# Kernel tuning notes

Measured on AMD Instinct MI355X. Metric: run time of the kernel, lower is better.

## Reference

```python
import jax, jax.numpy as jnp
import numpy as np

T = 2048          # tokens (flattened prefill)
H = 3584          # hidden_size
NH = 16           # num query heads
NKV = 8           # num kv heads
G = NH // NKV     # GQA group size
D = 256           # head_dim
SCALE = 256.0 ** -0.5   # query_pre_attn_scalar ** -0.5
WINDOW = 1024     # sliding_window_size
CAP = 50.0        # logit softcap
BASE = 10000.0    # rope theta
NEG = -1e30


def _rope(x, positions):
    # x: [T, n, D], neox-style rotary over full head_dim
    half = D // 2
    inv_freq = 1.0 / (BASE ** (jnp.arange(0, D, 2, dtype=jnp.float32) / D))  # [half]
    ang = positions.astype(jnp.float32)[:, None] * inv_freq  # [T, half]
    cos = jnp.cos(ang)[:, None, :]  # [T,1,half]
    sin = jnp.sin(ang)[:, None, :]
    x1, x2 = x[..., :half], x[..., half:]
    return jnp.concatenate([x1 * cos - x2 * sin, x2 * cos + x1 * sin], axis=-1)


def setup_inputs() -> dict:
    key = jax.random.key(0)
    ks = jax.random.split(key, 5)
    s = 0.02
    return {
        "hidden_states": jax.random.normal(ks[0], (T, H), dtype=jnp.float32),
        "Wq": jax.random.normal(ks[1], (H, NH * D), dtype=jnp.float32) * s,
        "Wk": jax.random.normal(ks[2], (H, NKV * D), dtype=jnp.float32) * s,
        "Wv": jax.random.normal(ks[3], (H, NKV * D), dtype=jnp.float32) * s,
        "Wo": jax.random.normal(ks[4], (NH * D, H), dtype=jnp.float32) * s,
        "positions": jnp.arange(T, dtype=jnp.int32),
    }


def reference(hidden_states, Wq, Wk, Wv, Wo, positions):
    q = (hidden_states @ Wq).reshape(T, NH, D)
    k = (hidden_states @ Wk).reshape(T, NKV, D)
    v = (hidden_states @ Wv).reshape(T, NKV, D)
    q = _rope(q, positions)
    k = _rope(k, positions)

    # GQA attention: group query heads over kv heads
    qg = (q * SCALE).reshape(T, NKV, G, D)
    scores = jnp.einsum('qhgd,khd->hgqk', qg, k)  # [NKV,G,T,T]
    scores = CAP * jnp.tanh(scores / CAP)         # logit softcap

    i = jnp.arange(T)[:, None]
    j = jnp.arange(T)[None, :]
    mask = (j <= i) & (i - j < WINDOW)            # causal + sliding window
    scores = jnp.where(mask, scores, NEG)

    p = jax.nn.softmax(scores, axis=-1)
    o = jnp.einsum('hgqk,khd->qhgd', p, v).reshape(T, NH * D)
    return o @ Wo
```

## Files before the change

kernel.cpp:

```cpp
#include <hip/hip_runtime.h>
#include <math.h>

typedef __attribute__((ext_vector_type(8))) __bf16 bf16x8;
typedef __attribute__((ext_vector_type(4))) __bf16 bf16x4;
typedef __attribute__((ext_vector_type(4))) float f32x4;

#define TSEQ 2048
#define HDIM 3584
#define NQH  16
#define NKVH 8
#define DH   256
#define WIN  1024
#define QKD  (NQH * DH)
#define KVD  (NKVH * DH)
#define QKVN 8192

#define MFMA __builtin_amdgcn_mfma_f32_16x16x32_bf16

__device__ __forceinline__ void gload_lds16(const void* g, void* l) {
  __builtin_amdgcn_global_load_lds(
      (const __attribute__((address_space(1))) void*)g,
      (__attribute__((address_space(3))) void*)l, 16, 0, 0);
}


__global__ void cvt_bf16_kernel(const float* __restrict__ in,
                                __bf16* __restrict__ out, long n) {
  long i = ((long)blockIdx.x * blockDim.x + threadIdx.x) * 4;
  if (i >= n) return;
  float4 v = *reinterpret_cast<const float4*>(in + i);
  bf16x4 o4;
  o4.x = (__bf16)v.x; o4.y = (__bf16)v.y; o4.z = (__bf16)v.z; o4.w = (__bf16)v.w;
  *reinterpret_cast<bf16x4*>(out + i) = o4;
}

__global__ void transpose_cvt_kernel(const float* __restrict__ in,
                                     __bf16* __restrict__ out, int R, int C) {
  __shared__ float tile[32][33];
  const int tx = threadIdx.x, ty = threadIdx.y;
  const int c0 = blockIdx.x * 32, r0 = blockIdx.y * 32;
#pragma unroll
  for (int i = 0; i < 4; ++i)
    tile[ty + i * 8][tx] = in[(size_t)(r0 + ty + i * 8) * C + (c0 + tx)];
  __syncthreads();
#pragma unroll
  for (int i = 0; i < 4; ++i)
    out[(size_t)(c0 + ty + i * 8) * R + (r0 + tx)] = (__bf16)tile[tx][ty + i * 8];
}

__global__ void transpose_bf16_kernel(const __bf16* __restrict__ in,
                                      __bf16* __restrict__ out, int ldin, int ldout) {
  __shared__ __bf16 tile[32][33];
  const int tx = threadIdx.x, ty = threadIdx.y;
  const int c0 = blockIdx.x * 32, r0 = blockIdx.y * 32;
#pragma unroll
  for (int i = 0; i < 4; ++i)
    tile[ty + i * 8][tx] = in[(size_t)(r0 + ty + i * 8) * ldin + (c0 + tx)];
  __syncthreads();
#pragma unroll
  for (int i = 0; i < 4; ++i)
    out[(size_t)(c0 + ty + i * 8) * ldout + (r0 + tx)] = tile[tx][ty + i * 8];
}

__global__ void rope_table_kernel(const int* __restrict__ positions,
                                  float* __restrict__ ct,
                                  float* __restrict__ st) {
  int i = blockIdx.x * blockDim.x + threadIdx.x;
  if (i >= TSEQ * 128) return;
  int t = i >> 7, j = i & 127;
  float invf = (float)exp((double)(-2 * j) * (9.210340371976184 / 256.0));
  float ang = (float)positions[t] * invf;
  ct[i] = cosf(ang);
  st[i] = sinf(ang);
}

__global__ void rope_apply_kernel(__bf16* __restrict__ x,
                                  const float* __restrict__ ct,
                                  const float* __restrict__ st,
                                  int heads, int ld, float scale, int total) {
  int i = blockIdx.x * blockDim.x + threadIdx.x;
  if (i >= total) return;
  int j = i & 127;
  int th = i >> 7;
  int t = th / heads;
  int head = th - t * heads;
  size_t base = (size_t)t * ld + head * DH + j;
  float x1 = (float)x[base], x2 = (float)x[base + 128];
  float c = ct[(t << 7) + j], s = st[(t << 7) + j];
  x[base]       = (__bf16)((x1 * c - x2 * s) * scale);
  x[base + 128] = (__bf16)((x2 * c + x1 * s) * scale);
}

__global__ void reduce2_kernel(const float* __restrict__ p0,
                               const float* __restrict__ p1,
                               float* __restrict__ out, int n4) {
  int stride = gridDim.x * blockDim.x;
  for (int i = blockIdx.x * blockDim.x + threadIdx.x; i < n4; i += stride) {
    float4 a = reinterpret_cast<const float4*>(p0)[i];
    float4 b = reinterpret_cast<const float4*>(p1)[i];
    a.x += b.x; a.y += b.y; a.z += b.z; a.w += b.w;
    reinterpret_cast<float4*>(out)[i] = a;
  }
}


__device__ __forceinline__ void stage_half(const __bf16* __restrict__ gbase,
                                           int row0, int ldg, int k0,
                                           __bf16* lds_half, int tid) {
  const int lane = tid & 63;
  const int w = tid >> 6;
  const int lr = lane >> 3;
  const int swzcol = ((lane & 7) ^ lr) << 3;
  const __bf16* g = gbase + (size_t)(row0 + w * 8 + lr) * ldg + k0 + swzcol;
  __bf16* l = lds_half + w * 512;
  gload_lds16(g, l);
  gload_lds16(g + (size_t)64 * ldg, l + 4096);
}

#define BAR __builtin_amdgcn_s_barrier()

#define RD_A(DST, BASE, MO)                                         \
  _Pragma("unroll")                                                 \
  for (int m_ = 0; m_ < 4; ++m_) {                                  \
    const __bf16* p_ = (BASE) + (((MO) + m_) * 16 + l15) * 64;      \
    DST[m_][0] = *(const bf16x8*)(p_ + kxa);                        \
    DST[m_][1] = *(const bf16x8*)(p_ + kxb);                        \
  }

#define RD_B(DST, BASE, NO)                                         \
  _Pragma("unroll")                                                 \
  for (int n_ = 0; n_ < 2; ++n_) {                                  \
    const __bf16* p_ = (BASE) + (bro + ((NO) + n_) * 16 + l15) * 64;\
    DST[n_][0] = *(const bf16x8*)(p_ + kxa);                        \
    DST[n_][1] = *(const bf16x8*)(p_ + kxb);                        \
  }

#define MQUAD(AF, BF, MO, NO)                                          \
  __builtin_amdgcn_s_setprio(1);                                       \
  _Pragma("unroll")                                                    \
  for (int m_ = 0; m_ < 4; ++m_)                                       \
    _Pragma("unroll")                                                  \
    for (int n_ = 0; n_ < 2; ++n_) {                                   \
      acc[(MO) + m_][(NO) + n_] =                                      \
          MFMA(AF[m_][0], BF[n_][0], acc[(MO) + m_][(NO) + n_], 0, 0, 0); \
      acc[(MO) + m_][(NO) + n_] =                                      \
          MFMA(AF[m_][1], BF[n_][1], acc[(MO) + m_][(NO) + n_], 0, 0, 0); \
    }                                                                  \
  __builtin_amdgcn_s_setprio(0);

template <typename CT>
__global__ __launch_bounds__(512, 2) void gemm256_kernel(
    const __bf16* __restrict__ A, const __bf16* __restrict__ B,
    CT* __restrict__ C, int lda, int Klen, int ldc, int nrc, size_t cstride) {
  __shared__ __bf16 lds[2][2][2][8192];

  const int nwg = gridDim.x;
  const int per = nwg >> 3;
  const int wg = (blockIdx.x & 7) * per + (blockIdx.x >> 3);
  const int kslice = wg / nrc;
  const int rem = wg - kslice * nrc;
  const int row0 = (rem & 7) * 256;
  const int col0 = (rem >> 3) * 256;
  const int k0 = kslice * Klen;
  CT* Cs = C + (size_t)kslice * cstride;

  const int tid = threadIdx.x;
  const int lane = tid & 63, w = tid >> 6;
  const int wr = w >> 2, wc = w & 3;
  const int l15 = lane & 15, lg = lane >> 4;
  const int swz = (lane & 7) << 3;
  const int kxa = (lg * 8) ^ swz;
  const int kxb = (32 + lg * 8) ^ swz;
  const int bro = (wc & 1) * 64;

  const __bf16* Ablk = A + (size_t)row0 * lda + k0;
  const __bf16* Bblk = B + (size_t)col0 * lda + k0;

  const __bf16* Ae = &lds[0][0][wr][0];
  const __bf16* Be = &lds[0][1][wc >> 1][0];
  const __bf16* Ao = &lds[1][0][wr][0];
  const __bf16* Bo = &lds[1][1][wc >> 1][0];

  f32x4 acc[8][4] = {};
  const int NT = Klen >> 6;
  const int NI = NT >> 1;

  stage_half(Ablk, 0,   lda, 0,  &lds[0][0][0][0], tid);
  stage_half(Ablk, 128, lda, 0,  &lds[0][0][1][0], tid);
  stage_half(Bblk, 0,   lda, 0,  &lds[0][1][0][0], tid);
  stage_half(Bblk, 128, lda, 0,  &lds[0][1][1][0], tid);
  stage_half(Ablk, 0,   lda, 64, &lds[1][0][0][0], tid);
  stage_half(Ablk, 128, lda, 64, &lds[1][0][1][0], tid);
  asm volatile("s_waitcnt vmcnt(4)" ::: "memory");
  BAR;

  bf16x8 a03[4][2], a47[4][2], b01[2][2], b23[2][2];

  for (int j = 0; j < NI; ++j) {
    const int e = 2 * j, o = 2 * j + 1;
    const bool last = (j == NI - 1);

    RD_A(a03, Ae, 0);
    RD_B(b01, Be, 0);
    stage_half(Bblk, 0, lda, o * 64, &lds[1][1][0][0], tid);
    asm volatile("s_waitcnt lgkmcnt(8)" ::: "memory");
    BAR; MQUAD(a03, b01, 0, 0); BAR;

    RD_A(a47, Ae, 4);
    stage_half(Bblk, 128, lda, o * 64, &lds[1][1][1][0], tid);
    BAR; MQUAD(a47, b01, 4, 0); BAR;

    RD_B(b23, Be, 2);
    if (!last) stage_half(Ablk, 0, lda, (e + 2) * 64, &lds[0][0][0][0], tid);
    BAR; MQUAD(a47, b23, 4, 2); BAR;

    if (!last) {
      stage_half(Ablk, 128, lda, (e + 2) * 64, &lds[0][0][1][0], tid);
      asm volatile("s_waitcnt vmcnt(4)" ::: "memory");
    } else {
      asm volatile("s_waitcnt vmcnt(0)" ::: "memory");
    }
    BAR; MQUAD(a03, b23, 0, 2); BAR;

    RD_A(a03, Ao, 0);
    RD_B(b01, Bo, 0);
    if (!last) stage_half(Bblk, 0, lda, (e + 2) * 64, &lds[0][1][0][0], tid);
    asm volatile("s_waitcnt lgkmcnt(8)" ::: "memory");
    BAR; MQUAD(a03, b01, 0, 0); BAR;

    RD_A(a47, Ao, 4);
    if (!last) stage_half(Bblk, 128, lda, (e + 2) * 64, &lds[0][1][1][0], tid);
    BAR; MQUAD(a47, b01, 4, 0); BAR;

    RD_B(b23, Bo, 2);
    if (!last) stage_half(Ablk, 0, lda, (o + 2) * 64, &lds[1][0][0][0], tid);
    BAR; MQUAD(a47, b23, 4, 2); BAR;

    if (!last) {
      stage_half(Ablk, 128, lda, (o + 2) * 64, &lds[1][0][1][0], tid);
      asm volatile("s_waitcnt vmcnt(4)" ::: "memory");
    }
    BAR; MQUAD(a03, b23, 0, 2); BAR;
  }

#pragma unroll
  for (int m = 0; m < 8; ++m)
#pragma unroll
    for (int n = 0; n < 4; ++n)
#pragma unroll
      for (int r = 0; r < 4; ++r) {
        int row = row0 + wr * 128 + m * 16 + lg * 4 + r;
        int col = col0 + wc * 64 + n * 16 + l15;
        Cs[(size_t)row * ldc + col] = (CT)acc[m][n][r];
      }
}

__global__ __launch_bounds__(256, 2) void attn_kernel(
    const __bf16* __restrict__ q, const __bf16* __restrict__ k,
    const __bf16* __restrict__ vt, __bf16* __restrict__ o) {
  __shared__ __bf16 Klds[64][264];
  __shared__ __bf16 Vlds[256][72];
  __shared__ __bf16 Plds[4][16][72];

  const int tid = threadIdx.x;
  const int wave = tid >> 6;
  const int lane = tid & 63;
  const int l16 = lane & 15;
  const int lg = lane >> 4;
  const int qh = blockIdx.y;
  const int h = qh >> 1;
  const int q0 = blockIdx.x << 6;
  const int qr = q0 + wave * 16;

  bf16x8 qf[8];
  {
    const __bf16* qp = q + (size_t)(qr + l16) * QKVN + qh * DH + lg * 8;
#pragma unroll
    for (int ds = 0; ds < 8; ++ds)
      qf[ds] = *reinterpret_cast<const bf16x8*>(qp + ds * 32);
  }

  f32x4 accO[16] = {};
  float l_run[4] = {0.f, 0.f, 0.f, 0.f};

  int t_lo = q0 - (WIN - 1);
  if (t_lo < 0) t_lo = 0;
  t_lo &= ~63;

  for (int t0 = t_lo; t0 <= q0; t0 += 64) {
    __syncthreads();
    {
      const __bf16* kg = k + (size_t)t0 * QKVN + h * DH;
#pragma unroll
      for (int it = 0; it < 8; ++it) {
        int c = tid + it * 256;
        int row = c >> 5, col = (c & 31) * 8;
        *reinterpret_cast<bf16x8*>(&Klds[row][col]) =
            *reinterpret_cast<const bf16x8*>(kg + (size_t)row * QKVN + col);
      }
      const __bf16* vg = vt + (size_t)(h * DH) * TSEQ + t0;
#pragma unroll
      for (int it = 0; it < 8; ++it) {
        int c = tid + it * 256;
        int row = c >> 3, col = (c & 7) * 8;
        *reinterpret_cast<bf16x8*>(&Vlds[row][col]) =
            *reinterpret_cast<const bf16x8*>(vg + (size_t)row * TSEQ + col);
      }
    }
    __syncthreads();

    f32x4 accS[4] = {};
    __builtin_amdgcn_s_setprio(1);
#pragma unroll
    for (int nt = 0; nt < 4; ++nt)
#pragma unroll
      for (int ds = 0; ds < 8; ++ds) {
        bf16x8 kf = *reinterpret_cast<const bf16x8*>(&Klds[nt * 16 + l16][ds * 32 + lg * 8]);
        accS[nt] = MFMA(qf[ds], kf, accS[nt], 0, 0, 0);
      }
    __builtin_amdgcn_s_setprio(0);

    float rs[4] = {0.f, 0.f, 0.f, 0.f};
#pragma unroll
    for (int nt = 0; nt < 4; ++nt) {
      int key = t0 + nt * 16 + l16;
#pragma unroll
      for (int r = 0; r < 4; ++r) {
        int row = qr + lg * 4 + r;
        float t = __expf(accS[nt][r] * 0.04f);
        float p = __expf(-100.0f / (t + 1.0f));
        bool valid = (key <= row) && (row - key < WIN);
        p = valid ? p : 0.f;
        rs[r] += p;
        Plds[wave][lg * 4 + r][nt * 16 + l16] = (__bf16)p;
      }
    }
#pragma unroll
    for (int off = 1; off < 16; off <<= 1)
#pragma unroll
      for (int r = 0; r < 4; ++r)
        rs[r] += __shfl_xor(rs[r], off);
#pragma unroll
    for (int r = 0; r < 4; ++r)
      l_run[r] += rs[r];

    __builtin_amdgcn_s_setprio(1);
#pragma unroll
    for (int ks = 0; ks < 2; ++ks) {
      bf16x8 pa = *reinterpret_cast<const bf16x8*>(&Plds[wave][l16][ks * 32 + lg * 8]);
#pragma unroll
      for (int nt2 = 0; nt2 < 16; ++nt2) {
        bf16x8 vb = *reinterpret_cast<const bf16x8*>(&Vlds[nt2 * 16 + l16][ks * 32 + lg * 8]);
        accO[nt2] = MFMA(pa, vb, accO[nt2], 0, 0, 0);
      }
    }
    __builtin_amdgcn_s_setprio(0);
  }

#pragma unroll
  for (int r = 0; r < 4; ++r) {
    float inv_l = 1.f / l_run[r];
    int row = qr + lg * 4 + r;
#pragma unroll
    for (int nt2 = 0; nt2 < 16; ++nt2)
      o[(size_t)row * QKD + qh * DH + nt2 * 16 + l16] = (__bf16)(accO[nt2][r] * inv_l);
  }
}


extern "C" void kernel_launch(void* const* d_in, const int* in_sizes, int n_in,
                              void* d_out, int out_size, void* d_ws, size_t ws_size,
                              hipStream_t stream) {
  const float* hs = (const float*)d_in[0];
  const float* Wq = (const float*)d_in[1];
  const float* Wk = (const float*)d_in[2];
  const float* Wv = (const float*)d_in[3];
  const float* Wo = (const float*)d_in[4];
  const int* positions = (const int*)d_in[5];
  float* out = (float*)d_out;

  char* ws = (char*)d_ws;
  const size_t SZ_HS  = (size_t)TSEQ * HDIM * 2;
  const size_t SZ_WQT = (size_t)QKD * HDIM * 2;
  const size_t SZ_WKT = (size_t)KVD * HDIM * 2;
  const size_t SZ_WOT = (size_t)HDIM * QKD * 2;
  const size_t SZ_QKV = (size_t)TSEQ * QKVN * 2;
  const size_t SZ_O   = (size_t)TSEQ * QKD * 2;
  const size_t SZ_TBL = (size_t)TSEQ * 128 * 4;

  __bf16* hs_bf = (__bf16*)ws; ws += SZ_HS;
  __bf16* WqT   = (__bf16*)ws; ws += SZ_WQT;
  __bf16* WkT   = (__bf16*)ws; ws += SZ_WKT;
  __bf16* WvT   = (__bf16*)ws; ws += SZ_WKT;
  __bf16* WoT   = (__bf16*)ws; ws += SZ_WOT;
  __bf16* qkv   = (__bf16*)ws; ws += SZ_QKV;
  __bf16* o_bf  = (__bf16*)ws; ws += SZ_O;
  float*  cost  = (float*)ws;  ws += SZ_TBL;
  float*  sint  = (float*)ws;  ws += SZ_TBL;
  __bf16* vt_bf = hs_bf;
  float* cpart = (float*)WqT;
  if ((size_t)(ws - (char*)d_ws) > ws_size) return;

  cvt_bf16_kernel<<<(TSEQ * HDIM) / 1024, 256, 0, stream>>>(hs, hs_bf, (long)TSEQ * HDIM);
  transpose_cvt_kernel<<<dim3(QKD / 32, HDIM / 32), dim3(32, 8), 0, stream>>>(Wq, WqT, HDIM, QKD);
  transpose_cvt_kernel<<<dim3(KVD / 32, HDIM / 32), dim3(32, 8), 0, stream>>>(Wk, WkT, HDIM, KVD);
  transpose_cvt_kernel<<<dim3(KVD / 32, HDIM / 32), dim3(32, 8), 0, stream>>>(Wv, WvT, HDIM, KVD);
  transpose_cvt_kernel<<<dim3(HDIM / 32, QKD / 32), dim3(32, 8), 0, stream>>>(Wo, WoT, QKD, HDIM);
  rope_table_kernel<<<(TSEQ * 128) / 256, 256, 0, stream>>>(positions, cost, sint);

  gemm256_kernel<__bf16><<<256, 512, 0, stream>>>(hs_bf, WqT, qkv, HDIM, HDIM, QKVN, 256, 0);

  rope_apply_kernel<<<(TSEQ * NQH * 128) / 256, 256, 0, stream>>>(qkv, cost, sint, NQH, QKVN, 0.0625f, TSEQ * NQH * 128);
  rope_apply_kernel<<<(TSEQ * NKVH * 128) / 256, 256, 0, stream>>>(qkv + QKD, cost, sint, NKVH, QKVN, 1.0f, TSEQ * NKVH * 128);
  transpose_bf16_kernel<<<dim3(KVD / 32, TSEQ / 32), dim3(32, 8), 0, stream>>>(qkv + QKD + KVD, vt_bf, QKVN, TSEQ);

  attn_kernel<<<dim3(TSEQ / 64, NQH), 256, 0, stream>>>(qkv, qkv + QKD, vt_bf, o_bf);

  gemm256_kernel<float><<<224, 512, 0, stream>>>(o_bf, WoT, cpart, QKD, QKD / 2, HDIM, 112,
                                                 (size_t)TSEQ * HDIM);
  reduce2_kernel<<<1792, 256, 0, stream>>>(cpart, cpart + (size_t)TSEQ * HDIM, out,
                                           TSEQ * HDIM / 4);
}
```

Baseline: 340.5 us.

## Share K/V tiles across GQA query heads, prefetch next tile, widen weight transpose

The attention kernel now runs one block per KV head with 512 threads, so both query heads of a GQA group reuse the same K/V LDS tiles instead of loading them twice. It also prefetches the next K/V tile into registers while computing on the current one. The weight transpose-convert kernel switches to 64x64 tiles with float4 loads and 8-wide bf16 stores. The grid has half as many attention blocks, and the 512-thread launch bound plus the extra prefetch registers may limit occupancy.

```diff
diff --git a/kernel.cpp b/kernel.cpp
--- a/kernel.cpp
+++ b/kernel.cpp
@@ -34,18 +34,29 @@
   *reinterpret_cast<bf16x4*>(out + i) = o4;
 }
 
-__global__ void transpose_cvt_kernel(const float* __restrict__ in,
-                                     __bf16* __restrict__ out, int R, int C) {
-  __shared__ float tile[32][33];
-  const int tx = threadIdx.x, ty = threadIdx.y;
-  const int c0 = blockIdx.x * 32, r0 = blockIdx.y * 32;
-#pragma unroll
-  for (int i = 0; i < 4; ++i)
-    tile[ty + i * 8][tx] = in[(size_t)(r0 + ty + i * 8) * C + (c0 + tx)];
+__global__ void transpose_cvt64_kernel(const float* __restrict__ in,
+                                       __bf16* __restrict__ out, int R, int C) {
+  __shared__ float tile[64][65];
+  const int tid = threadIdx.x;
+  const int r0 = blockIdx.y * 64, c0 = blockIdx.x * 64;
+#pragma unroll
+  for (int it = 0; it < 4; ++it) {
+    int f = tid + it * 256;
+    int row = f >> 4, c4 = (f & 15) * 4;
+    float4 v = *reinterpret_cast<const float4*>(&in[(size_t)(r0 + row) * C + c0 + c4]);
+    tile[row][c4] = v.x; tile[row][c4 + 1] = v.y;
+    tile[row][c4 + 2] = v.z; tile[row][c4 + 3] = v.w;
+  }
   __syncthreads();
 #pragma unroll
-  for (int i = 0; i < 4; ++i)
-    out[(size_t)(c0 + ty + i * 8) * R + (r0 + tx)] = (__bf16)tile[tx][ty + i * 8];
+  for (int it = 0; it < 2; ++it) {
+    int s = tid + it * 256;
+    int oc = s >> 3, rb = (s & 7) * 8;
+    bf16x8 o8;
+#pragma unroll
+    for (int j = 0; j < 8; ++j) o8[j] = (__bf16)tile[rb + j][oc];
+    *reinterpret_cast<bf16x8*>(&out[(size_t)(c0 + oc) * R + r0 + rb]) = o8;
+  }
 }
 
 __global__ void transpose_bf16_kernel(const __bf16* __restrict__ in,
@@ -255,22 +266,23 @@
       }
 }
 
-__global__ __launch_bounds__(256, 2) void attn_kernel(
+__global__ __launch_bounds__(512, 2) void attn_kernel(
     const __bf16* __restrict__ q, const __bf16* __restrict__ k,
     const __bf16* __restrict__ vt, __bf16* __restrict__ o) {
   __shared__ __bf16 Klds[64][264];
   __shared__ __bf16 Vlds[256][72];
-  __shared__ __bf16 Plds[4][16][72];
+  __shared__ __bf16 Plds[8][16][72];
 
   const int tid = threadIdx.x;
   const int wave = tid >> 6;
   const int lane = tid & 63;
   const int l16 = lane & 15;
   const int lg = lane >> 4;
-  const int qh = blockIdx.y;
-  const int h = qh >> 1;
+  const int h = blockIdx.y;
+  const int qh = 2 * h + (wave >> 2);
+  const int wsub = wave & 3;
   const int q0 = blockIdx.x << 6;
-  const int qr = q0 + wave * 16;
+  const int qr = q0 + wsub * 16;
 
   bf16x8 qf[8];
   {
@@ -287,27 +299,40 @@
   if (t_lo < 0) t_lo = 0;
   t_lo &= ~63;
 
+  const __bf16* kg0 = k + (size_t)h * DH;
+  const __bf16* vg0 = vt + (size_t)(h * DH) * TSEQ;
+
+  bf16x8 kpre[4], vpre[4];
+#pragma unroll
+  for (int it = 0; it < 4; ++it) {
+    int c = tid + it * 512;
+    kpre[it] = *reinterpret_cast<const bf16x8*>(
+        kg0 + (size_t)(t_lo + (c >> 5)) * QKVN + (c & 31) * 8);
+    vpre[it] = *reinterpret_cast<const bf16x8*>(
+        vg0 + (size_t)(c >> 3) * TSEQ + t_lo + (c & 7) * 8);
+  }
+
   for (int t0 = t_lo; t0 <= q0; t0 += 64) {
     __syncthreads();
-    {
-      const __bf16* kg = k + (size_t)t0 * QKVN + h * DH;
-#pragma unroll
-      for (int it = 0; it < 8; ++it) {
-        int c = tid + it * 256;
-        int row = c >> 5, col = (c & 31) * 8;
-        *reinterpret_cast<bf16x8*>(&Klds[row][col]) =
-            *reinterpret_cast<const bf16x8*>(kg + (size_t)row * QKVN + col);
+#pragma unroll
+    for (int it = 0; it < 4; ++it) {
+      int c = tid + it * 512;
+      *reinterpret_cast<bf16x8*>(&Klds[c >> 5][(c & 31) * 8]) = kpre[it];
+      *reinterpret_cast<bf16x8*>(&Vlds[c >> 3][(c & 7) * 8]) = vpre[it];
+    }
+    __syncthreads();
+
+    if (t0 + 64 <= q0) {
+      const int tn = t0 + 64;
+#pragma unroll
+      for (int it = 0; it < 4; ++it) {
+        int c = tid + it * 512;
+        kpre[it] = *reinterpret_cast<const bf16x8*>(
+            kg0 + (size_t)(tn + (c >> 5)) * QKVN + (c & 31) * 8);
+        vpre[it] = *reinterpret_cast<const bf16x8*>(
+            vg0 + (size_t)(c >> 3) * TSEQ + tn + (c & 7) * 8);
       }
-      const __bf16* vg = vt + (size_t)(h * DH) * TSEQ + t0;
-#pragma unroll
-      for (int it = 0; it < 8; ++it) {
-        int c = tid + it * 256;
-        int row = c >> 3, col = (c & 7) * 8;
-        *reinterpret_cast<bf16x8*>(&Vlds[row][col]) =
-            *reinterpret_cast<const bf16x8*>(vg + (size_t)row * TSEQ + col);
-      }
-    }
-    __syncthreads();
+    }
 
     f32x4 accS[4] = {};
     __builtin_amdgcn_s_setprio(1);
@@ -402,10 +427,10 @@
   if ((size_t)(ws - (char*)d_ws) > ws_size) return;
 
   cvt_bf16_kernel<<<(TSEQ * HDIM) / 1024, 256, 0, stream>>>(hs, hs_bf, (long)TSEQ * HDIM);
-  transpose_cvt_kernel<<<dim3(QKD / 32, HDIM / 32), dim3(32, 8), 0, stream>>>(Wq, WqT, HDIM, QKD);
-  transpose_cvt_kernel<<<dim3(KVD / 32, HDIM / 32), dim3(32, 8), 0, stream>>>(Wk, WkT, HDIM, KVD);
-  transpose_cvt_kernel<<<dim3(KVD / 32, HDIM / 32), dim3(32, 8), 0, stream>>>(Wv, WvT, HDIM, KVD);
-  transpose_cvt_kernel<<<dim3(HDIM / 32, QKD / 32), dim3(32, 8), 0, stream>>>(Wo, WoT, QKD, HDIM);
+  transpose_cvt64_kernel<<<dim3(QKD / 64, HDIM / 64), 256, 0, stream>>>(Wq, WqT, HDIM, QKD);
+  transpose_cvt64_kernel<<<dim3(KVD / 64, HDIM / 64), 256, 0, stream>>>(Wk, WkT, HDIM, KVD);
+  transpose_cvt64_kernel<<<dim3(KVD / 64, HDIM / 64), 256, 0, stream>>>(Wv, WvT, HDIM, KVD);
+  transpose_cvt64_kernel<<<dim3(HDIM / 64, QKD / 64), 256, 0, stream>>>(Wo, WoT, QKD, HDIM);
   rope_table_kernel<<<(TSEQ * 128) / 256, 256, 0, stream>>>(positions, cost, sint);
 
   gemm256_kernel<__bf16><<<256, 512, 0, stream>>>(hs_bf, WqT, qkv, HDIM, HDIM, QKVN, 256, 0);
@@ -414,7 +439,7 @@
   rope_apply_kernel<<<(TSEQ * NKVH * 128) / 256, 256, 0, stream>>>(qkv + QKD, cost, sint, NKVH, QKVN, 1.0f, TSEQ * NKVH * 128);
   transpose_bf16_kernel<<<dim3(KVD / 32, TSEQ / 32), dim3(32, 8), 0, stream>>>(qkv + QKD + KVD, vt_bf, QKVN, TSEQ);
 
-  attn_kernel<<<dim3(TSEQ / 64, NQH), 256, 0, stream>>>(qkv, qkv + QKD, vt_bf, o_bf);
+  attn_kernel<<<dim3(TSEQ / 64, NKVH), 512, 0, stream>>>(qkv, qkv + QKD, vt_bf, o_bf);
 
   gemm256_kernel<float><<<224, 512, 0, stream>>>(o_bf, WoT, cpart, QKD, QKD / 2, HDIM, 112,
                                                  (size_t)TSEQ * HDIM);
```

New measurement: 336.2 us. Within noise of the previous version (-1.3%).
